# Kernel tuning notes

Measured on AMD Instinct MI355X. Metric: run time of the kernel, lower is better.

The kernel has to match this reference:

```python
import jax, jax.numpy as jnp
import numpy as np

NUM_HEADS = 32
NUM_KV_HEADS = 8
HEAD_DIM = 128
SCALE = 0.08838834764831845  # head_dim ** -0.5
LENS = [1024, 900, 800, 700, 600, 500, 400, 300]  # ragged sequence lengths


def setup_inputs() -> dict:
    key = jax.random.key(0)
    kq, kk, kv = jax.random.split(key, 3)
    cu = np.concatenate([[0], np.cumsum(LENS)]).astype(np.int32)
    T = int(cu[-1])  # 5224 total tokens
    q = jax.random.normal(kq, (T, NUM_HEADS * HEAD_DIM), jnp.float32)
    k = jax.random.normal(kk, (T, NUM_KV_HEADS * HEAD_DIM), jnp.float32)
    v = jax.random.normal(kv, (T, NUM_KV_HEADS * HEAD_DIM), jnp.float32)
    return {"q": q, "k": k, "v": v, "cu_seqlens": jnp.asarray(cu), "max_seqlen": 1024}


def _varlen_indices(cu_seqlens, total_tokens):
    # For each flat token, which sequence it belongs to and its position within it.
    pos = jnp.arange(total_tokens)
    seq_idx = jnp.searchsorted(cu_seqlens[1:], pos, side='right')
    pos_idx = pos - cu_seqlens[seq_idx]
    return seq_idx, pos_idx


def reference(q, k, v, cu_seqlens, max_seqlen):
    T = q.shape[0]
    B = cu_seqlens.shape[0] - 1
    q = q.reshape(T, NUM_HEADS, HEAD_DIM)
    k = k.reshape(T, NUM_KV_HEADS, HEAD_DIM)
    v = v.reshape(T, NUM_KV_HEADS, HEAD_DIM)
    si, pi = _varlen_indices(cu_seqlens, T)

    # varlen -> padded [B, L, H, D] (scatter)
    def pad(x):
        return jnp.zeros((B, max_seqlen) + x.shape[1:], x.dtype).at[si, pi].set(x)

    qp, kp, vp = pad(q), pad(k), pad(v)

    # GQA: repeat_interleave KV heads to match query heads
    rep = NUM_HEADS // NUM_KV_HEADS
    kp = jnp.repeat(kp, rep, axis=2)
    vp = jnp.repeat(vp, rep, axis=2)

    # causal SDPA on padded tensors
    scores = jnp.einsum('bihd,bjhd->bhij', qp, kp) * SCALE  # [B,H,L,L]
    causal = jnp.tril(jnp.ones((max_seqlen, max_seqlen), bool))
    scores = jnp.where(causal, scores, -jnp.inf)
    attn = jax.nn.softmax(scores, axis=-1)
    op = jnp.einsum('bhij,bjhd->bihd', attn, vp)  # [B,L,H,D]

    # padded -> varlen [T, H, D] (gather)
    return op[si, pi]
```

## Files before the change

### kernel.cpp

```cpp
#include <hip/hip_runtime.h>
#include <math.h>

#define NUM_HEADS 32
#define NUM_KV_HEADS 8
#define HEAD_DIM 128
#define QSTRIDE 4096
#define KSTRIDE 1024
#define SCALE 0.08838834764831845f
#define BM 128
#define BN 64
#define PSP 72
#define K1C (SCALE * 1.4426950408889634f)
#define K2C (6.0f * 1.4426950408889634f)

typedef __attribute__((ext_vector_type(8))) short short8;
typedef __attribute__((ext_vector_type(16))) float floatx16;

__device__ __forceinline__ ushort f2bf(float f) {
  union { float f; unsigned u; } x; x.f = f;
  unsigned r = x.u + 0x7fffu + ((x.u >> 16) & 1u);
  return (ushort)(r >> 16);
}

__device__ __forceinline__ void async16(ushort* lds, const ushort* g) {
  __builtin_amdgcn_global_load_lds(
      (const __attribute__((address_space(1))) unsigned*)g,
      (__attribute__((address_space(3))) unsigned*)lds, 16, 0, 0);
}

__global__ __launch_bounds__(256)
void prep_k(const float* __restrict__ k, ushort* __restrict__ kb, long n) {
  long i = ((long)blockIdx.x * 256 + threadIdx.x) * 8;
  if (i >= n) return;
  float4 a = *(const float4*)(k + i);
  float4 b = *(const float4*)(k + i + 4);
  ushort w[8] = {f2bf(a.x), f2bf(a.y), f2bf(a.z), f2bf(a.w),
                 f2bf(b.x), f2bf(b.y), f2bf(b.z), f2bf(b.w)};
  *(short8*)(kb + i) = *(short8*)w;
}

__global__ __launch_bounds__(256)
void prep_v(const float* __restrict__ v, ushort* __restrict__ vt, int T, int Tpad) {
  const int kt = blockIdx.x * 64;
  const int kvh = blockIdx.y;
  __shared__ __align__(16) ushort Ls[128][PSP];
  const int j = threadIdx.x >> 2;
  const int dc = (threadIdx.x & 3) * 32;
  const int t = kt + j;
  const int pj = (j & 31) * 2 + (j >> 5);
  const float* gv = v + (size_t)t * KSTRIDE + kvh * HEAD_DIM + dc;
  #pragma unroll
  for (int i = 0; i < 32; i += 4) {
    float4 x = (t < T) ? *(const float4*)(gv + i) : make_float4(0.f, 0.f, 0.f, 0.f);
    Ls[dc + i + 0][pj] = f2bf(x.x);
    Ls[dc + i + 1][pj] = f2bf(x.y);
    Ls[dc + i + 2][pj] = f2bf(x.z);
    Ls[dc + i + 3][pj] = f2bf(x.w);
  }
  __syncthreads();
  const int d = threadIdx.x >> 1;
  const int k0 = (threadIdx.x & 1) * 32;
  ushort* g = vt + (size_t)(kvh * HEAD_DIM + d) * Tpad + kt + k0;
  #pragma unroll
  for (int i = 0; i < 32; i += 8)
    *(short8*)(g + i) = *(short8*)&Ls[d][k0 + i];
}

__global__ __launch_bounds__(256, 2)
void fa_kernel(const float* __restrict__ q, const ushort* __restrict__ kb,
               const ushort* __restrict__ vt, const int* __restrict__ cu,
               float* __restrict__ out, int T, int Tpad, int B, int nt) {
  const int tid = threadIdx.x;
  const int wave = tid >> 6;
  const int lane = tid & 63;
  const int l32 = lane & 31;
  const int half = lane >> 5;
  const int xr = l32 & 7;
  const int h = blockIdx.y;
  const int kvh = h >> 2;
  const int tile = nt - 1 - blockIdx.x;
  const int row0 = tile * BM;

  __shared__ __align__(16) ushort KsL[64 * 128];
  __shared__ __align__(16) ushort VtL[128 * 64];
  __shared__ __align__(16) ushort PsL[4 * 32 * PSP];
  __shared__ int rstart[BM], rtok[BM];

  if (tid < BM) {
    int t = row0 + tid;
    int st = 0, tkk = -1;
    if (t < T) {
      int s = 0;
      while (s < B - 1 && cu[s + 1] <= t) s++;
      st = cu[s]; tkk = t;
    }
    rstart[tid] = st; rtok[tid] = tkk;
  }

  short8 aq[8];
  {
    int myrow = row0 + wave * 32 + l32;
    if (myrow < T) {
      const float* gq = q + (size_t)myrow * QSTRIDE + h * HEAD_DIM + half * 8;
      #pragma unroll
      for (int s = 0; s < 8; s++) {
        float4 x = *(const float4*)(gq + s * 16);
        float4 y = *(const float4*)(gq + s * 16 + 4);
        ushort w[8] = {f2bf(x.x), f2bf(x.y), f2bf(x.z), f2bf(x.w),
                       f2bf(y.x), f2bf(y.y), f2bf(y.z), f2bf(y.w)};
        aq[s] = *(short8*)w;
      }
    } else {
      #pragma unroll
      for (int s = 0; s < 8; s++) aq[s] = (short8){0, 0, 0, 0, 0, 0, 0, 0};
    }
  }
  __syncthreads();

  int rs[16], tk[16];
  #pragma unroll
  for (int r = 0; r < 16; r++) {
    int qr = (r & 3) + 8 * (r >> 2) + 4 * half;
    rs[r] = rstart[wave * 32 + qr];
    tk[r] = rtok[wave * 32 + qr];
  }

  size_t koff[4], voff[4];
  ushort *kdst[4], *vdst[4];
  #pragma unroll
  for (int i = 0; i < 4; i++) {
    int c = wave * 4 + i;
    int r = c * 4 + (lane >> 4);
    int js = lane & 15;
    int j = (js & 8) | ((js ^ (r & 7)) & 7);
    koff[i] = (size_t)r * KSTRIDE + kvh * HEAD_DIM + j * 8;
    kdst[i] = KsL + c * 512;
    int d = c * 8 + (lane >> 3);
    int js2 = lane & 7;
    int j2 = js2 ^ (d & 7);
    voff[i] = (size_t)(kvh * HEAD_DIM + d) * Tpad + j2 * 8;
    vdst[i] = VtL + c * 512;
  }

  floatx16 o0 = {0.f,0.f,0.f,0.f,0.f,0.f,0.f,0.f,0.f,0.f,0.f,0.f,0.f,0.f,0.f,0.f};
  floatx16 o1 = o0, o2 = o0, o3 = o0, lsum = o0;
  const short8 vones = {16256,16256,16256,16256,16256,16256,16256,16256};

  const int kt0 = (rstart[0] / BN) * BN;
  const int tmax = min(row0 + BM - 1, T - 1);

  ushort* psw = PsL + wave * (32 * PSP) + half * (4 * PSP) + l32 * 2;
  const ushort* psr = PsL + wave * (32 * PSP) + l32 * PSP + half * 8;

  for (int kt = kt0; kt <= tmax; kt += BN) {
    __syncthreads();
    #pragma unroll
    for (int i = 0; i < 4; i++) async16(kdst[i], kb + (size_t)kt * KSTRIDE + koff[i]);
    #pragma unroll
    for (int i = 0; i < 4; i++) async16(vdst[i], vt + voff[i] + kt);
    __syncthreads();

    floatx16 c0 = {0.f,0.f,0.f,0.f,0.f,0.f,0.f,0.f,0.f,0.f,0.f,0.f,0.f,0.f,0.f,0.f};
    floatx16 c1 = c0;
    #pragma unroll
    for (int s = 0; s < 8; s++) {
      int j = 2 * s + half;
      int jsw = (j & 8) | ((j ^ xr) & 7);
      const short8 b0 = *(const short8*)&KsL[l32 * 128 + jsw * 8];
      const short8 b1 = *(const short8*)&KsL[l32 * 128 + jsw * 8 + 4096];
      c0 = __builtin_amdgcn_mfma_f32_32x32x16_bf16(aq[s], b0, c0, 0, 0, 0);
      c1 = __builtin_amdgcn_mfma_f32_32x32x16_bf16(aq[s], b1, c1, 0, 0, 0);
    }

    const int kj0 = kt + l32, kj1 = kt + 32 + l32;
    #pragma unroll
    for (int r = 0; r < 16; r++) {
      bool v0 = (kj0 >= rs[r]) & (kj0 <= tk[r]);
      bool v1 = (kj1 >= rs[r]) & (kj1 <= tk[r]);
      float p0 = v0 ? __builtin_amdgcn_exp2f(fmaf(c0[r], K1C, -K2C)) : 0.f;
      float p1 = v1 ? __builtin_amdgcn_exp2f(fmaf(c1[r], K1C, -K2C)) : 0.f;
      unsigned pk = __builtin_amdgcn_perm(__float_as_uint(p1), __float_as_uint(p0),
                                          0x07060302u);
      *(unsigned*)(psw + ((r & 3) + 8 * (r >> 2)) * PSP) = pk;
    }

    #pragma unroll
    for (int ka = 0; ka < 4; ka++) {
      const short8 ap = *(const short8*)(psr + ka * 16);
      lsum = __builtin_amdgcn_mfma_f32_32x32x16_bf16(ap, vones, lsum, 0, 0, 0);
      int j2 = (2 * ka + half) ^ xr;
      const short8 bv0 = *(const short8*)&VtL[l32 * 64 + j2 * 8];
      const short8 bv1 = *(const short8*)&VtL[2048 + l32 * 64 + j2 * 8];
      const short8 bv2 = *(const short8*)&VtL[4096 + l32 * 64 + j2 * 8];
      const short8 bv3 = *(const short8*)&VtL[6144 + l32 * 64 + j2 * 8];
      o0 = __builtin_amdgcn_mfma_f32_32x32x16_bf16(ap, bv0, o0, 0, 0, 0);
      o1 = __builtin_amdgcn_mfma_f32_32x32x16_bf16(ap, bv1, o1, 0, 0, 0);
      o2 = __builtin_amdgcn_mfma_f32_32x32x16_bf16(ap, bv2, o2, 0, 0, 0);
      o3 = __builtin_amdgcn_mfma_f32_32x32x16_bf16(ap, bv3, o3, 0, 0, 0);
    }
  }

  #pragma unroll
  for (int r = 0; r < 16; r++) {
    if (tk[r] < 0) continue;
    float inv = 1.f / lsum[r];
    float* go = out + (size_t)tk[r] * QSTRIDE + h * HEAD_DIM + l32;
    go[0]  = o0[r] * inv;
    go[32] = o1[r] * inv;
    go[64] = o2[r] * inv;
    go[96] = o3[r] * inv;
  }
}

extern "C" void kernel_launch(void* const* d_in, const int* in_sizes, int n_in,
                              void* d_out, int out_size, void* d_ws, size_t ws_size,
                              hipStream_t stream) {
  const float* q = (const float*)d_in[0];
  const float* k = (const float*)d_in[1];
  const float* v = (const float*)d_in[2];
  const int* cu = (const int*)d_in[3];
  float* out = (float*)d_out;
  int T = in_sizes[0] / QSTRIDE;
  int B = in_sizes[3] - 1;
  int Tpad = ((T + 63) / 64) * 64;

  ushort* kb = (ushort*)d_ws;
  ushort* vt = kb + (size_t)Tpad * 1024;

  long nk = (long)T * KSTRIDE;
  hipLaunchKernelGGL(prep_k, dim3((unsigned)((nk / 8 + 255) / 256)), dim3(256), 0, stream,
                     k, kb, nk);
  hipLaunchKernelGGL(prep_v, dim3(Tpad / 64, NUM_KV_HEADS), dim3(256), 0, stream,
                     v, vt, T, Tpad);
  int nt = (T + BM - 1) / BM;
  hipLaunchKernelGGL(fa_kernel, dim3(nt, NUM_HEADS), dim3(256), 0, stream,
                     q, kb, vt, cu, out, T, Tpad, B, nt);
}
```

Baseline: 262.4 us.

## Double-buffer K/V tiles, keep P in registers, fuse prep kernels, reorder tile schedule

Merges the K and V conversion kernels into one launch. In the attention kernel, K/V tiles are now double-buffered in LDS with asynchronous prefetch of the next tile, and the score MFMA operands are swapped so P can be built in registers via cvt_pk_bf16 and permlane32_swap instead of a round-trip through LDS. Row sums are accumulated on the VALU instead of with an extra MFMA, fully unmasked tiles skip the mask checks, and the grid is reordered with a hardcoded tile permutation for nt=41 plus head interleaving for load balance. The changes add LDS use and register pressure, and the permutation is tuned to this specific token count.

After: 256.7 us. -2.2%, faster.

```diff
diff --git a/kernel.cpp b/kernel.cpp
--- a/kernel.cpp
+++ b/kernel.cpp
@@ -12,9 +12,17 @@
 #define PSP 72
 #define K1C (SCALE * 1.4426950408889634f)
 #define K2C (6.0f * 1.4426950408889634f)
+#define KHALF 8192
+#define VHALF 8192
 
 typedef __attribute__((ext_vector_type(8))) short short8;
 typedef __attribute__((ext_vector_type(16))) float floatx16;
+typedef __attribute__((ext_vector_type(4))) float f32x4;
+
+__constant__ unsigned char PERM41[41] = {
+  7, 15, 6, 14, 21, 5, 13, 20, 26, 31, 4, 12, 19, 25, 35, 30,
+  3, 11, 18, 24, 34, 38, 29, 2, 10, 17, 23, 33, 37, 40, 28,
+  1, 9, 16, 22, 32, 36, 39, 27, 0, 8};
 
 __device__ __forceinline__ ushort f2bf(float f) {
   union { float f; unsigned u; } x; x.f = f;
@@ -28,42 +36,53 @@
       (__attribute__((address_space(3))) unsigned*)lds, 16, 0, 0);
 }
 
+__device__ __forceinline__ unsigned cvtpk(float lo, float hi) {
+  unsigned r;
+  asm("v_cvt_pk_bf16_f32 %0, %1, %2" : "=v"(r) : "v"(lo), "v"(hi));
+  return r;
+}
+
 __global__ __launch_bounds__(256)
-void prep_k(const float* __restrict__ k, ushort* __restrict__ kb, long n) {
-  long i = ((long)blockIdx.x * 256 + threadIdx.x) * 8;
-  if (i >= n) return;
-  float4 a = *(const float4*)(k + i);
-  float4 b = *(const float4*)(k + i + 4);
-  ushort w[8] = {f2bf(a.x), f2bf(a.y), f2bf(a.z), f2bf(a.w),
-                 f2bf(b.x), f2bf(b.y), f2bf(b.z), f2bf(b.w)};
-  *(short8*)(kb + i) = *(short8*)w;
-}
-
-__global__ __launch_bounds__(256)
-void prep_v(const float* __restrict__ v, ushort* __restrict__ vt, int T, int Tpad) {
-  const int kt = blockIdx.x * 64;
-  const int kvh = blockIdx.y;
+void prep(const float* __restrict__ k, const float* __restrict__ v,
+          ushort* __restrict__ kb, ushort* __restrict__ vt,
+          int T, int Tpad, int kblk, long nkpad) {
   __shared__ __align__(16) ushort Ls[128][PSP];
-  const int j = threadIdx.x >> 2;
-  const int dc = (threadIdx.x & 3) * 32;
-  const int t = kt + j;
-  const int pj = (j & 31) * 2 + (j >> 5);
-  const float* gv = v + (size_t)t * KSTRIDE + kvh * HEAD_DIM + dc;
-  #pragma unroll
-  for (int i = 0; i < 32; i += 4) {
-    float4 x = (t < T) ? *(const float4*)(gv + i) : make_float4(0.f, 0.f, 0.f, 0.f);
-    Ls[dc + i + 0][pj] = f2bf(x.x);
-    Ls[dc + i + 1][pj] = f2bf(x.y);
-    Ls[dc + i + 2][pj] = f2bf(x.z);
-    Ls[dc + i + 3][pj] = f2bf(x.w);
-  }
-  __syncthreads();
-  const int d = threadIdx.x >> 1;
-  const int k0 = (threadIdx.x & 1) * 32;
-  ushort* g = vt + (size_t)(kvh * HEAD_DIM + d) * Tpad + kt + k0;
-  #pragma unroll
-  for (int i = 0; i < 32; i += 8)
-    *(short8*)(g + i) = *(short8*)&Ls[d][k0 + i];
+  if ((int)blockIdx.x < kblk) {
+    long i = ((long)blockIdx.x * 256 + threadIdx.x) * 8;
+    if (i >= nkpad) return;
+    long lim = (long)T * KSTRIDE;
+    ushort w[8] = {0, 0, 0, 0, 0, 0, 0, 0};
+    if (i < lim) {
+      float4 a = *(const float4*)(k + i);
+      float4 b = *(const float4*)(k + i + 4);
+      w[0] = f2bf(a.x); w[1] = f2bf(a.y); w[2] = f2bf(a.z); w[3] = f2bf(a.w);
+      w[4] = f2bf(b.x); w[5] = f2bf(b.y); w[6] = f2bf(b.z); w[7] = f2bf(b.w);
+    }
+    *(short8*)(kb + i) = *(short8*)w;
+  } else {
+    int vb = (int)blockIdx.x - kblk;
+    const int kt = (vb >> 3) * 64;
+    const int kvh = vb & 7;
+    const int j = threadIdx.x >> 2;
+    const int dc = (threadIdx.x & 3) * 32;
+    const int t = kt + j;
+    const float* gv = v + (size_t)t * KSTRIDE + kvh * HEAD_DIM + dc;
+    #pragma unroll
+    for (int i = 0; i < 32; i += 4) {
+      float4 x = (t < T) ? *(const float4*)(gv + i) : make_float4(0.f, 0.f, 0.f, 0.f);
+      Ls[dc + i + 0][j] = f2bf(x.x);
+      Ls[dc + i + 1][j] = f2bf(x.y);
+      Ls[dc + i + 2][j] = f2bf(x.z);
+      Ls[dc + i + 3][j] = f2bf(x.w);
+    }
+    __syncthreads();
+    const int d = threadIdx.x >> 1;
+    const int k0 = (threadIdx.x & 1) * 32;
+    ushort* g = vt + (size_t)(kvh * HEAD_DIM + d) * Tpad + kt + k0;
+    #pragma unroll
+    for (int i = 0; i < 32; i += 8)
+      *(short8*)(g + i) = *(short8*)&Ls[d][k0 + i];
+  }
 }
 
 __global__ __launch_bounds__(256, 2)
@@ -76,14 +95,13 @@
   const int l32 = lane & 31;
   const int half = lane >> 5;
   const int xr = l32 & 7;
-  const int h = blockIdx.y;
+  const int h = ((int)blockIdx.x & 7) * 4 + ((int)blockIdx.x >> 3);
   const int kvh = h >> 2;
-  const int tile = nt - 1 - blockIdx.x;
+  const int tile = (nt == 41) ? (int)PERM41[blockIdx.y] : (nt - 1 - (int)blockIdx.y);
   const int row0 = tile * BM;
 
-  __shared__ __align__(16) ushort KsL[64 * 128];
-  __shared__ __align__(16) ushort VtL[128 * 64];
-  __shared__ __align__(16) ushort PsL[4 * 32 * PSP];
+  __shared__ __align__(16) ushort KsL[2 * KHALF];
+  __shared__ __align__(16) ushort VtL[2 * VHALF];
   __shared__ int rstart[BM], rtok[BM];
 
   if (tid < BM) {
@@ -97,36 +115,8 @@
     rstart[tid] = st; rtok[tid] = tkk;
   }
 
-  short8 aq[8];
-  {
-    int myrow = row0 + wave * 32 + l32;
-    if (myrow < T) {
-      const float* gq = q + (size_t)myrow * QSTRIDE + h * HEAD_DIM + half * 8;
-      #pragma unroll
-      for (int s = 0; s < 8; s++) {
-        float4 x = *(const float4*)(gq + s * 16);
-        float4 y = *(const float4*)(gq + s * 16 + 4);
-        ushort w[8] = {f2bf(x.x), f2bf(x.y), f2bf(x.z), f2bf(x.w),
-                       f2bf(y.x), f2bf(y.y), f2bf(y.z), f2bf(y.w)};
-        aq[s] = *(short8*)w;
-      }
-    } else {
-      #pragma unroll
-      for (int s = 0; s < 8; s++) aq[s] = (short8){0, 0, 0, 0, 0, 0, 0, 0};
-    }
-  }
-  __syncthreads();
-
-  int rs[16], tk[16];
-  #pragma unroll
-  for (int r = 0; r < 16; r++) {
-    int qr = (r & 3) + 8 * (r >> 2) + 4 * half;
-    rs[r] = rstart[wave * 32 + qr];
-    tk[r] = rtok[wave * 32 + qr];
-  }
-
   size_t koff[4], voff[4];
-  ushort *kdst[4], *vdst[4];
+  int soff[4];
   #pragma unroll
   for (int i = 0; i < 4; i++) {
     int c = wave * 4 + i;
@@ -134,81 +124,132 @@
     int js = lane & 15;
     int j = (js & 8) | ((js ^ (r & 7)) & 7);
     koff[i] = (size_t)r * KSTRIDE + kvh * HEAD_DIM + j * 8;
-    kdst[i] = KsL + c * 512;
     int d = c * 8 + (lane >> 3);
-    int js2 = lane & 7;
-    int j2 = js2 ^ (d & 7);
+    int j2 = (lane & 7) ^ (d & 7);
     voff[i] = (size_t)(kvh * HEAD_DIM + d) * Tpad + j2 * 8;
-    vdst[i] = VtL + c * 512;
-  }
-
-  floatx16 o0 = {0.f,0.f,0.f,0.f,0.f,0.f,0.f,0.f,0.f,0.f,0.f,0.f,0.f,0.f,0.f,0.f};
-  floatx16 o1 = o0, o2 = o0, o3 = o0, lsum = o0;
-  const short8 vones = {16256,16256,16256,16256,16256,16256,16256,16256};
+    soff[i] = c * 512;
+  }
+
+  __syncthreads();
 
   const int kt0 = (rstart[0] / BN) * BN;
   const int tmax = min(row0 + BM - 1, T - 1);
-
-  ushort* psw = PsL + wave * (32 * PSP) + half * (4 * PSP) + l32 * 2;
-  const ushort* psr = PsL + wave * (32 * PSP) + l32 * PSP + half * 8;
-
-  for (int kt = kt0; kt <= tmax; kt += BN) {
-    __syncthreads();
-    #pragma unroll
-    for (int i = 0; i < 4; i++) async16(kdst[i], kb + (size_t)kt * KSTRIDE + koff[i]);
-    #pragma unroll
-    for (int i = 0; i < 4; i++) async16(vdst[i], vt + voff[i] + kt);
-    __syncthreads();
+  const int rs_q = rstart[wave * 32 + l32];
+  const int tk_q = rtok[wave * 32 + l32];
+
+  #pragma unroll
+  for (int i = 0; i < 4; i++) async16(KsL + soff[i], kb + (size_t)kt0 * KSTRIDE + koff[i]);
+  #pragma unroll
+  for (int i = 0; i < 4; i++) async16(VtL + soff[i], vt + voff[i] + kt0);
+
+  short8 aq[8];
+  {
+    int myrow = row0 + wave * 32 + l32;
+    if (myrow < T) {
+      const float* gq = q + (size_t)myrow * QSTRIDE + h * HEAD_DIM + half * 8;
+      #pragma unroll
+      for (int s = 0; s < 8; s++) {
+        f32x4 x = __builtin_nontemporal_load((const f32x4*)(gq + s * 16));
+        f32x4 y = __builtin_nontemporal_load((const f32x4*)(gq + s * 16 + 4));
+        ushort w[8] = {f2bf(x.x), f2bf(x.y), f2bf(x.z), f2bf(x.w),
+                       f2bf(y.x), f2bf(y.y), f2bf(y.z), f2bf(y.w)};
+        aq[s] = *(short8*)w;
+      }
+    } else {
+      #pragma unroll
+      for (int s = 0; s < 8; s++) aq[s] = (short8){0, 0, 0, 0, 0, 0, 0, 0};
+    }
+  }
+
+  floatx16 o0 = {0.f,0.f,0.f,0.f,0.f,0.f,0.f,0.f,0.f,0.f,0.f,0.f,0.f,0.f,0.f,0.f};
+  floatx16 o1 = o0, o2 = o0, o3 = o0;
+  float sm = 0.f;
+
+  __syncthreads();
+
+  int cur = 0;
+  for (int kt = kt0; kt <= tmax; kt += BN, cur ^= 1) {
+    const ushort* Ks = KsL + cur * KHALF;
+    const ushort* Vt = VtL + cur * VHALF;
+
+    int ktn = kt + BN;
+    if (ktn <= tmax) {
+      ushort* kd = KsL + (cur ^ 1) * KHALF;
+      ushort* vd = VtL + (cur ^ 1) * VHALF;
+      #pragma unroll
+      for (int i = 0; i < 4; i++) async16(kd + soff[i], kb + (size_t)ktn * KSTRIDE + koff[i]);
+      #pragma unroll
+      for (int i = 0; i < 4; i++) async16(vd + soff[i], vt + voff[i] + ktn);
+    }
 
     floatx16 c0 = {0.f,0.f,0.f,0.f,0.f,0.f,0.f,0.f,0.f,0.f,0.f,0.f,0.f,0.f,0.f,0.f};
     floatx16 c1 = c0;
+    __builtin_amdgcn_s_setprio(1);
     #pragma unroll
     for (int s = 0; s < 8; s++) {
       int j = 2 * s + half;
       int jsw = (j & 8) | ((j ^ xr) & 7);
-      const short8 b0 = *(const short8*)&KsL[l32 * 128 + jsw * 8];
-      const short8 b1 = *(const short8*)&KsL[l32 * 128 + jsw * 8 + 4096];
-      c0 = __builtin_amdgcn_mfma_f32_32x32x16_bf16(aq[s], b0, c0, 0, 0, 0);
-      c1 = __builtin_amdgcn_mfma_f32_32x32x16_bf16(aq[s], b1, c1, 0, 0, 0);
-    }
-
-    const int kj0 = kt + l32, kj1 = kt + 32 + l32;
-    #pragma unroll
-    for (int r = 0; r < 16; r++) {
-      bool v0 = (kj0 >= rs[r]) & (kj0 <= tk[r]);
-      bool v1 = (kj1 >= rs[r]) & (kj1 <= tk[r]);
-      float p0 = v0 ? __builtin_amdgcn_exp2f(fmaf(c0[r], K1C, -K2C)) : 0.f;
-      float p1 = v1 ? __builtin_amdgcn_exp2f(fmaf(c1[r], K1C, -K2C)) : 0.f;
-      unsigned pk = __builtin_amdgcn_perm(__float_as_uint(p1), __float_as_uint(p0),
-                                          0x07060302u);
-      *(unsigned*)(psw + ((r & 3) + 8 * (r >> 2)) * PSP) = pk;
-    }
-
-    #pragma unroll
-    for (int ka = 0; ka < 4; ka++) {
-      const short8 ap = *(const short8*)(psr + ka * 16);
-      lsum = __builtin_amdgcn_mfma_f32_32x32x16_bf16(ap, vones, lsum, 0, 0, 0);
-      int j2 = (2 * ka + half) ^ xr;
-      const short8 bv0 = *(const short8*)&VtL[l32 * 64 + j2 * 8];
-      const short8 bv1 = *(const short8*)&VtL[2048 + l32 * 64 + j2 * 8];
-      const short8 bv2 = *(const short8*)&VtL[4096 + l32 * 64 + j2 * 8];
-      const short8 bv3 = *(const short8*)&VtL[6144 + l32 * 64 + j2 * 8];
-      o0 = __builtin_amdgcn_mfma_f32_32x32x16_bf16(ap, bv0, o0, 0, 0, 0);
-      o1 = __builtin_amdgcn_mfma_f32_32x32x16_bf16(ap, bv1, o1, 0, 0, 0);
-      o2 = __builtin_amdgcn_mfma_f32_32x32x16_bf16(ap, bv2, o2, 0, 0, 0);
-      o3 = __builtin_amdgcn_mfma_f32_32x32x16_bf16(ap, bv3, o3, 0, 0, 0);
-    }
-  }
-
+      const short8 b0 = *(const short8*)&Ks[l32 * 128 + jsw * 8];
+      const short8 b1 = *(const short8*)&Ks[l32 * 128 + jsw * 8 + 4096];
+      c0 = __builtin_amdgcn_mfma_f32_32x32x16_bf16(b0, aq[s], c0, 0, 0, 0);
+      c1 = __builtin_amdgcn_mfma_f32_32x32x16_bf16(b1, aq[s], c1, 0, 0, 0);
+    }
+    __builtin_amdgcn_s_setprio(0);
+
+    const bool fullt = __all((rs_q <= kt) & (tk_q >= kt + BN - 1));
+
+    #pragma unroll
+    for (int g = 0; g < 4; g++) {
+      const floatx16& cc = (g < 2) ? c0 : c1;
+      const int r0 = (g & 1) * 8;
+      float p[8];
+      if (fullt) {
+        #pragma unroll
+        for (int jj = 0; jj < 8; jj++)
+          p[jj] = __builtin_amdgcn_exp2f(fmaf(cc[r0 + jj], K1C, -K2C));
+      } else {
+        int kbase = kt + 16 * g + 4 * half;
+        #pragma unroll
+        for (int jj = 0; jj < 8; jj++) {
+          int key = kbase + (jj & 3) + 8 * (jj >> 2);
+          bool vld = (key >= rs_q) & (key <= tk_q);
+          p[jj] = vld ? __builtin_amdgcn_exp2f(fmaf(cc[r0 + jj], K1C, -K2C)) : 0.f;
+        }
+      }
+      sm += ((p[0] + p[1]) + (p[2] + p[3])) + ((p[4] + p[5]) + (p[6] + p[7]));
+      unsigned w0 = cvtpk(p[0], p[1]);
+      unsigned w1 = cvtpk(p[2], p[3]);
+      unsigned w2 = cvtpk(p[4], p[5]);
+      unsigned w3 = cvtpk(p[6], p[7]);
+      asm("v_permlane32_swap_b32 %0, %1" : "+v"(w0), "+v"(w2));
+      asm("v_permlane32_swap_b32 %0, %1" : "+v"(w1), "+v"(w3));
+      union { unsigned u[4]; short8 s8; } ap;
+      ap.u[0] = w0; ap.u[1] = w1; ap.u[2] = w2; ap.u[3] = w3;
+      int j2 = (2 * g + half) ^ xr;
+      const ushort* Vb = Vt + l32 * 64 + j2 * 8;
+      o0 = __builtin_amdgcn_mfma_f32_32x32x16_bf16(ap.s8, *(const short8*)(Vb), o0, 0, 0, 0);
+      o1 = __builtin_amdgcn_mfma_f32_32x32x16_bf16(ap.s8, *(const short8*)(Vb + 2048), o1, 0, 0, 0);
+      o2 = __builtin_amdgcn_mfma_f32_32x32x16_bf16(ap.s8, *(const short8*)(Vb + 4096), o2, 0, 0, 0);
+      o3 = __builtin_amdgcn_mfma_f32_32x32x16_bf16(ap.s8, *(const short8*)(Vb + 6144), o3, 0, 0, 0);
+    }
+
+    __syncthreads();
+  }
+
+  float smT = sm + __shfl_xor(sm, 32, 64);
   #pragma unroll
   for (int r = 0; r < 16; r++) {
-    if (tk[r] < 0) continue;
-    float inv = 1.f / lsum[r];
-    float* go = out + (size_t)tk[r] * QSTRIDE + h * HEAD_DIM + l32;
-    go[0]  = o0[r] * inv;
-    go[32] = o1[r] * inv;
-    go[64] = o2[r] * inv;
-    go[96] = o3[r] * inv;
+    int qr = (r & 3) + 8 * (r >> 2) + 4 * half;
+    float dn = __shfl(smT, qr, 64);
+    int tkr = rtok[wave * 32 + qr];
+    if (tkr >= 0) {
+      float inv = 1.f / dn;
+      float* go = out + (size_t)tkr * QSTRIDE + h * HEAD_DIM + l32;
+      __builtin_nontemporal_store(o0[r] * inv, go);
+      __builtin_nontemporal_store(o1[r] * inv, go + 32);
+      __builtin_nontemporal_store(o2[r] * inv, go + 64);
+      __builtin_nontemporal_store(o3[r] * inv, go + 96);
+    }
   }
 }
 
@@ -227,12 +268,12 @@
   ushort* kb = (ushort*)d_ws;
   ushort* vt = kb + (size_t)Tpad * 1024;
 
-  long nk = (long)T * KSTRIDE;
-  hipLaunchKernelGGL(prep_k, dim3((unsigned)((nk / 8 + 255) / 256)), dim3(256), 0, stream,
-                     k, kb, nk);
-  hipLaunchKernelGGL(prep_v, dim3(Tpad / 64, NUM_KV_HEADS), dim3(256), 0, stream,
-                     v, vt, T, Tpad);
+  long nkpad = (long)Tpad * KSTRIDE;
+  int kblk = (int)((nkpad / 8 + 255) / 256);
+  int vblk = (Tpad / 64) * NUM_KV_HEADS;
+  hipLaunchKernelGGL(prep, dim3(kblk + vblk), dim3(256), 0, stream,
+                     k, v, kb, vt, T, Tpad, kblk, nkpad);
   int nt = (T + BM - 1) / BM;
-  hipLaunchKernelGGL(fa_kernel, dim3(nt, NUM_HEADS), dim3(256), 0, stream,
+  hipLaunchKernelGGL(fa_kernel, dim3(NUM_HEADS, nt), dim3(256), 0, stream,
                      q, kb, vt, cu, out, T, Tpad, B, nt);
 }
```
